# Kernel optimization log

Hardware: AMD Instinct MI355X
Metric: run time of the kernel (lower is better)

## Reference

```python
import jax, jax.numpy as jnp
import numpy as np
from jax import lax

PI = 3.14159265
# (dh, dw) for each of the 8 discretized angle bins, matching the torch `direction` table
DIRS = jnp.array([[1, 0], [1, 1], [0, 1], [-1, 1], [-1, 0], [-1, -1], [0, -1], [1, -1]], dtype=jnp.int32)
CC_ITERS = 48  # fixed trip count; FastSV converges in O(log N) rounds (log2(512*512)=18)


def _grids(H, W):
    return jnp.meshgrid(jnp.arange(H, dtype=jnp.int32), jnp.arange(W, dtype=jnp.int32), indexing='ij')


def _find_parents(angles, theta_a):
    # vectorized version of find_parents: per-pixel angle bin -> neighbor; root if OOB or angle gap too large
    H, W = angles.shape
    ii, jj = _grids(H, W)
    pos = jnp.round((angles + PI / 8.0) / (PI / 4.0))
    pos = jnp.where(pos >= 8.0, pos - 8.0, pos).astype(jnp.int32)
    nh = ii + DIRS[pos, 0]
    nw = jj + DIRS[pos, 1]
    inb = (nh >= 0) & (nh < H) & (nw >= 0) & (nw < W)
    nhc = jnp.clip(nh, 0, H - 1)
    nwc = jnp.clip(nw, 0, W - 1)
    ad = jnp.abs(angles - angles[nhc, nwc])
    ad = jnp.minimum(ad, 2.0 * PI - ad)
    is_root = (~inb) | (ad > theta_a * PI / 180.0)
    ph = jnp.where(is_root, ii, nhc)
    pw = jnp.where(is_root, jj, nwc)
    return ph, pw, is_root


def _cc_min_label(u, v, n):
    # Parallel union-find with min-label semantics (FastSV: root hooking + pointer jumping).
    # Equivalent to the serial UNION/FIND: final label of each pixel = min pixel index in its component.
    f0 = jnp.arange(n, dtype=jnp.int32)

    def body(_, f):
        fu, fv = f[u], f[v]
        m = jnp.minimum(fu, fv)
        g = f.at[fu].min(m).at[fv].min(m).at[u].min(m).at[v].min(m)
        g = g[g]
        g = g[g]
        return g

    return lax.fori_loop(0, CC_ITERS, body, f0)


def _structures(angles, theta_a):
    # All integer / discrete structure: parents, union-find labels, 3-step ancestors, boundary masks.
    H, W = angles.shape
    N = H * W
    ii, jj = _grids(H, W)
    ph, pw, roots = _find_parents(angles, theta_a)
    pf = (ph * W + pw).reshape(-1)  # flat parent pointer per pixel
    idx = jnp.arange(N, dtype=jnp.int32)
    # stage-1 edges: pixel <-> parent; stage-2 edges: merge_nearby_root_pixels window
    # range(0, min(3, H-1-i)) x range(-min(3, j), min(3, W-1-j))  <=>  dh in {0,1,2} with nh<=H-2,
    # dw in {-3..2} with 0<=nw<=W-2, both endpoints roots
    us, vs = [idx], [pf]
    for dh in range(0, 3):
        for dw in range(-3, 3):
            nh, nw = ii + dh, jj + dw
            nhc = jnp.clip(nh, 0, H - 1)
            nwc = jnp.clip(nw, 0, W - 1)
            m = roots & (nh <= H - 2) & (nw >= 0) & (nw <= W - 2) & roots[nhc, nwc]
            us.append(jnp.where(m, ii * W + jj, 0).reshape(-1))
            vs.append(jnp.where(m, nhc * W + nwc, 0).reshape(-1))
    labels_after = _cc_min_label(jnp.concatenate(us), jnp.concatenate(vs), N) + 1  # super_BPDs after dilation
    c3 = pf[pf[pf]]  # 3-step parent chase for every pixel (as in find_bnd_angle_diff)
    # boundary masks for right (0,1) and down (1,0) neighbors
    masks, nidxs = [], []
    for dh, dw in ((0, 1), (1, 0)):
        nh, nw = ii + dh, jj + dw
        valid = ((nh < H) & (nw < W)).reshape(-1)
        nidx = (jnp.clip(nh, 0, H - 1) * W + jnp.clip(nw, 0, W - 1)).reshape(-1)
        masks.append(valid & (labels_after != labels_after[nidx]))
        nidxs.append(nidx)
    return c3, masks, nidxs


def _bnd_angle_diff(angles, c3, masks, nidxs):
    # per boundary pixel-pair: wrap-around angle difference of the two 3-step ancestors
    H, W = angles.shape
    ang = angles.reshape(-1)
    outs = []
    for mask, nidx in zip(masks, nidxs):
        ad = jnp.abs(ang[c3] - ang[c3[nidx]])
        ad = jnp.minimum(ad, 2.0 * PI - ad)
        outs.append(jnp.where(mask, ad, 0.0))
    return jnp.stack(outs, axis=-1).reshape(H, W, 2)


def setup_inputs():
    key = jax.random.key(0)
    H, W = 512, 512
    input_angles = jax.random.uniform(key, (H, W), jnp.float32, 0.0, 2.0 * PI)
    return {"input_angles": input_angles, "height": H, "width": W, "theta_a": 45, "S_o": 90}


def reference(input_angles, height, width, theta_a, S_o):
    c3, masks, nidxs = _structures(input_angles, theta_a)
    return _bnd_angle_diff(input_angles, c3, masks, nidxs)
```

## Files before the change

### kernel.cpp

```cpp
#include <hip/hip_runtime.h>


static constexpr double PI_D = 3.14159265;
#define LCAP 4096
#define EPT  256
#define MAXT 1024

__device__ __constant__ int c_DH[8] = {1, 1, 0, -1, -1, -1, 0, 1};
__device__ __constant__ int c_DW[8] = {0, 1, 1, 1, 0, -1, -1, -1};

__device__ int g_fb[4 * 262144 + (MAXT << 10) + 2 * MAXT + 2 * EPT * MAXT];

__device__ __forceinline__ int uf_find_lds(int x, int* par) {
    while (true) {
        int p = par[x];
        if (p == x) return x;
        int gp = par[p];
        if (gp == p) return p;
        atomicMin(&par[x], gp);
        x = gp;
    }
}
__device__ __forceinline__ void uf_unite_lds(int u, int v, int* par) {
    int ru = uf_find_lds(u, par);
    int rv = uf_find_lds(v, par);
    while (ru != rv) {
        if (ru > rv) { int t2 = ru; ru = rv; rv = t2; }
        int old = atomicMin(&par[rv], ru);
        if (old == rv) break;
        rv = uf_find_lds(old, par);
        ru = uf_find_lds(ru, par);
    }
}

__device__ __forceinline__ int find_ro(int x, const int* par) {
    int p = par[x];
    while (p != x) { x = p; p = par[x]; }
    return x;
}
__device__ __forceinline__ void uf_unite(int u, int v, int* par) {
    int ru = find_ro(u, par);
    int rv = find_ro(v, par);
    while (ru != rv) {
        if (ru > rv) { int t2 = ru; ru = rv; rv = t2; }
        int old = atomicMin(&par[rv], ru);
        if (old == rv) break;
        rv = find_ro(old, par);
        ru = find_ro(ru, par);
    }
}

__device__ __forceinline__ bool parent_dir(const float* __restrict__ ang, float a,
                                           int i, int j, int H, int W, float thr,
                                           int& nhc, int& nwc) {
    const float a8 = (float)(PI_D / 8.0);
    const float a4 = (float)(PI_D / 4.0);
    float posf = rintf((a + a8) / a4);
    if (posf >= 8.0f) posf -= 8.0f;
    const int pos = (int)posf;
    const int nh = i + c_DH[pos];
    const int nw = j + c_DW[pos];
    const bool inb = (nh >= 0) & (nh < H) & (nw >= 0) & (nw < W);
    nhc = min(max(nh, 0), H - 1);
    nwc = min(max(nw, 0), W - 1);
    float ad = fabsf(a - ang[nhc * W + nwc]);
    const float twopi = (float)(2.0 * PI_D);
    ad = fminf(ad, twopi - ad);
    return (!inb) || (ad > thr);
}

__global__ void __launch_bounds__(1024)
k_local(const float* __restrict__ ang,
        const int* __restrict__ hp, const int* __restrict__ wp,
        const int* __restrict__ tap, int N,
        int* __restrict__ pf, int* __restrict__ par, int* __restrict__ c3,
        int* __restrict__ wlist, int* __restrict__ idx, int* __restrict__ wcnt) {
    const int H = hp[0], W = wp[0];
    const float thr = (float)((double)tap[0] * PI_D / 180.0);
    const int tpr = (W + 31) >> 5;
    const int ntiles = tpr * ((H + 31) >> 5);
    __shared__ int lpar[1024];
    __shared__ int lpl[1024];
    __shared__ int scnt;
    const int lp = threadIdx.x;
    const int li = lp >> 5, lj = lp & 31;
    for (int tile = blockIdx.x; tile < ntiles; tile += gridDim.x) {
        const int ti0 = (tile / tpr) << 5, tj0 = (tile % tpr) << 5;
        const int i = ti0 + li, j = tj0 + lj;
        const bool inpix = (i < H) && (j < W);
        const int g = i * W + j;
        if (lp == 0) scnt = 0;
        lpar[lp] = lp;
        int lparent = lp;
        if (inpix) {
            int nh, nw;
            const bool root = parent_dir(ang, ang[g], i, j, H, W, thr, nh, nw);
            pf[g] = root ? g : (nh * W + nw);
            if (!root) {
                const int pli = nh - ti0, plj = nw - tj0;
                lparent = (((unsigned)pli < 32u) && ((unsigned)plj < 32u))
                              ? ((pli << 5) + plj) : -1;
            }
        }
        lpl[lp] = lparent;
        __syncthreads();
        if (inpix) {
            if (lparent != lp) {
                if (lparent >= 0) uf_unite_lds(lp, lparent, lpar);
            } else if (i <= H - 2) {
                for (int d = 1; d <= 3; ++d) {
                    if (lj + d > 31 || j + d > W - 1) break;
                    if (lpl[lp + d] == lp + d) { uf_unite_lds(lp, lp + d, lpar); break; }
                }
                for (int dh = 1; dh <= 2; ++dh) {
                    const int nh = i + dh;
                    if (nh > H - 2) break;
                    const int nli = li + dh;
                    if (nli >= 32) break;
                    for (int dw = -3; dw <= 2; ++dw) {
                        const int nw = j + dw;
                        if ((unsigned)nw > (unsigned)(W - 2)) continue;
                        const int nlj = lj + dw;
                        if ((unsigned)nlj > 31u) continue;
                        const int nlp = (nli << 5) + nlj;
                        if (lpl[nlp] == nlp) uf_unite_lds(lp, nlp, lpar);
                    }
                }
            }
        }
        __syncthreads();
        if (inpix) {
            const int lr = uf_find_lds(lp, lpar);
            par[g] = (ti0 + (lr >> 5)) * W + (tj0 + (lr & 31));
            if (lr == lp) {
                const int s = atomicAdd(&scnt, 1);
                wlist[(tile << 10) + s] = g;
                idx[g] = s;
            }
            if (li >= 3 && li <= 28 && lj >= 3 && lj <= 28) {
                int v = lpl[lp];
                v = lpl[v];
                v = lpl[v];
                c3[g] = (ti0 + (v >> 5)) * W + (tj0 + (v & 31));
            }
        }
        __syncthreads();
        if (lp == 0) wcnt[tile] = scnt;
        __syncthreads();
    }
}

__global__ void k_edges(const int* __restrict__ pf,
                        const int* __restrict__ hp, const int* __restrict__ wp,
                        int N, int* par, int* __restrict__ elist, int* __restrict__ ecnt) {
    const int H = hp[0], W = wp[0];
    const int tpr = (W + 31) >> 5;
    const int ntiles = tpr * ((H + 31) >> 5);
    const int tidx = threadIdx.x;
    __shared__ unsigned long long htab[256];
    __shared__ int scnt;
    int li = 0, lj = 0;
    if (tidx < 96) {
        const int r = tidx >> 5;
        li = (r == 0) ? 0 : 29 + r;
        lj = tidx & 31;
    } else if (tidx < 270) {
        const int u = tidx - 96;
        li = 1 + u / 6;
        const int c = u % 6;
        lj = (c < 3) ? c : 26 + c;
    }
    for (int tile = blockIdx.x; tile < ntiles; tile += gridDim.x) {
        for (int s = tidx; s < 256; s += blockDim.x) htab[s] = ~0ull;
        if (tidx == 0) scnt = 0;
        __syncthreads();
        const int i = ((tile / tpr) << 5) + li;
        const int j = ((tile % tpr) << 5) + lj;
        if (tidx < 270 && i < H && j < W) {
            const int t = i * W + j;
            auto EMIT = [&](int a, int b) {
                if (a == b) return;
                const int lo = min(a, b), hi2 = max(a, b);
                const unsigned long long key =
                    ((unsigned long long)lo << 20) | (unsigned)hi2;
                unsigned h = (unsigned)((key * 0x9E3779B97F4A7C15ull) >> 52) & 255u;
                bool fresh = true;
                for (int pr = 0; pr < 16; ++pr) {
                    unsigned long long old = atomicCAS(&htab[h], ~0ull, key);
                    if (old == ~0ull) break;
                    if (old == key) { fresh = false; break; }
                    h = (h + 1) & 255u;
                }
                if (!fresh) return;
                const int s = atomicAdd(&scnt, 1);
                if (s < EPT) {
                    elist[(tile * EPT + s) * 2] = lo;
                    elist[(tile * EPT + s) * 2 + 1] = hi2;
                } else {
                    uf_unite(lo, hi2, par);
                }
            };
            const int p = pf[t];
            if (p != t) {
                const int pi = p / W, pj = p - pi * W;
                if (((pi ^ i) | (pj ^ j)) & ~31) EMIT(par[t], par[p]);
            } else if (i <= H - 2) {
                const int pt = par[t];
                int h0 = -1, h1 = -1;
                for (int d = (lj >= 29 ? 32 - lj : 4); d <= 3; ++d) {
                    if (j + d > W - 1) break;
                    const int n = t + d;
                    if (pf[n] != n) continue;
                    const int pn = par[n];
                    if (pn == pt || pn == h0 || pn == h1) continue;
                    h1 = h0; h0 = pn;
                    EMIT(pt, pn);
                }
                for (int dh = 1; dh <= 2; ++dh) {
                    const int nh = i + dh;
                    if (nh > H - 2) break;
                    const bool rowcross = (li + dh) > 31;
                    for (int dw = -3; dw <= 2; ++dw) {
                        const int nw = j + dw;
                        if ((unsigned)nw > (unsigned)(W - 2)) continue;
                        if (!rowcross && ((unsigned)(lj + dw) <= 31u)) continue;
                        const int n = nh * W + nw;
                        if (pf[n] != n) continue;
                        const int pn = par[n];
                        if (pn == pt || pn == h0 || pn == h1) continue;
                        h1 = h0; h0 = pn;
                        EMIT(pt, pn);
                    }
                }
            }
        }
        __syncthreads();
        if (tidx == 0) ecnt[tile] = scnt;
        __syncthreads();
    }
}

__global__ void __launch_bounds__(1024)
k_merge(const int* __restrict__ wlist, const int* __restrict__ wcnt,
        const int* __restrict__ idx, const int* __restrict__ elist,
        const int* __restrict__ ecnt,
        const int* __restrict__ hp, const int* __restrict__ wp, int* par) {
    const int H = hp[0], W = wp[0];
    const int tpr = (W + 31) >> 5;
    const int ntiles = tpr * ((H + 31) >> 5);
    __shared__ int lpar[LCAP], pix[LCAP], mn[LCAP];
    __shared__ int base[MAXT + 1], ebase[MAXT + 1];
    __shared__ int nsh, esh;
    const int tid = threadIdx.x;
    for (int t = tid; t < ntiles; t += blockDim.x) {
        base[t] = wcnt[t];
        ebase[t] = min(ecnt[t], EPT);
    }
    __syncthreads();
    if (tid == 0) {
        int rn = 0, re = 0;
        for (int t = 0; t < ntiles; ++t) {
            int c = base[t];  base[t] = rn;  rn += c;
            int e = ebase[t]; ebase[t] = re; re += e;
        }
        base[ntiles] = rn;  ebase[ntiles] = re;
        nsh = rn; esh = re;
    }
    __syncthreads();
    const int n = nsh, E = esh;
    auto bsearch = [&](const int* pre, int k) {
        int lo = 0, hi = ntiles;
        while (hi - lo > 1) { int m = (lo + hi) >> 1; if (pre[m] <= k) lo = m; else hi = m; }
        return lo;
    };
    auto CID = [&](int px) {
        const int pi = px / W, pj = px - pi * W;
        return base[(pi >> 5) * tpr + (pj >> 5)] + idx[px];
    };
    if (n <= LCAP) {
        for (int k = tid; k < n; k += blockDim.x) {
            const int t = bsearch(base, k);
            const int px = wlist[(t << 10) + (k - base[t])];
            pix[k] = px; lpar[k] = k; mn[k] = px;
        }
        __syncthreads();
        for (int k = tid; k < n; k += blockDim.x) {
            const int px = pix[k];
            const int q = par[px];
            if (q != px) uf_unite_lds(k, CID(q), lpar);
        }
        for (int e = tid; e < E; e += blockDim.x) {
            const int t = bsearch(ebase, e);
            const int s = e - ebase[t];
            const int a = elist[(t * EPT + s) * 2];
            const int b = elist[(t * EPT + s) * 2 + 1];
            uf_unite_lds(CID(a), CID(b), lpar);
        }
        __syncthreads();
        for (int k = tid; k < n; k += blockDim.x) {
            const int r = uf_find_lds(k, lpar);
            if (r != k) atomicMin(&mn[r], pix[k]);
        }
        __syncthreads();
        for (int k = tid; k < n; k += blockDim.x)
            par[pix[k]] = mn[uf_find_lds(k, lpar)];
    } else {
        for (int e = tid; e < E; e += blockDim.x) {
            const int t = bsearch(ebase, e);
            const int s = e - ebase[t];
            uf_unite(elist[(t * EPT + s) * 2], elist[(t * EPT + s) * 2 + 1], par);
        }
        __syncthreads();
        for (int k = tid; k < n; k += blockDim.x) {
            const int t = bsearch(base, k);
            const int r = wlist[(t << 10) + (k - base[t])];
            par[r] = find_ro(r, par);
        }
    }
}

__global__ void __launch_bounds__(256)
k_output(const float* __restrict__ ang,
         const int* __restrict__ par, const int* __restrict__ pf,
         const int* __restrict__ c3,
         const int* __restrict__ hp, const int* __restrict__ wp,
         float* __restrict__ out) {
    const int H = hp[0], W = wp[0];
    const int i0 = blockIdx.y << 3;
    const int j0 = blockIdx.x << 5;
    __shared__ int lab[9][33];
    const int tid = threadIdx.x;
    for (int k = tid; k < 9 * 33; k += 256) {
        const int r = k / 33, c = k - r * 33;
        const int gi = min(i0 + r, H - 1), gj = min(j0 + c, W - 1);
        lab[r][c] = par[par[gi * W + gj]];
    }
    __syncthreads();
    const int li2 = tid >> 5, lj2 = tid & 31;
    const int i = i0 + li2, j = j0 + lj2;
    if (i >= H || j >= W) return;
    const int t = i * W + j;
    const float twopi = (float)(2.0 * PI_D);
    const int l = lab[li2][lj2];
    float r0 = 0.0f, r1 = 0.0f;
    bool need = false;
    int l1 = l, l2 = l;
    if (j + 1 < W) { l1 = lab[li2][lj2 + 1]; need |= (l1 != l); }
    if (i + 1 < H) { l2 = lab[li2 + 1][lj2]; need |= (l2 != l); }
    if (need) {
        auto c3v = [&](int x, int xli, int xlj) {
            if (xli >= 3 && xli <= 28 && xlj >= 3 && xlj <= 28) return c3[x];
            int p = pf[x];
            p = pf[p];
            return pf[p];
        };
        const float ac = ang[c3v(t, i & 31, j & 31)];
        if (l1 != l) {
            float ad = fabsf(ac - ang[c3v(t + 1, i & 31, (j + 1) & 31)]);
            r0 = fminf(ad, twopi - ad);
        }
        if (l2 != l) {
            float ad = fabsf(ac - ang[c3v(t + W, (i + 1) & 31, j & 31)]);
            r1 = fminf(ad, twopi - ad);
        }
    }
    reinterpret_cast<float2*>(out)[t] = make_float2(r0, r1);
}

extern "C" void kernel_launch(void* const* d_in, const int* in_sizes, int n_in,
                              void* d_out, int out_size, void* d_ws, size_t ws_size,
                              hipStream_t stream) {
    const float* ang = (const float*)d_in[0];
    const int* hp  = (const int*)d_in[1];
    const int* wp  = (const int*)d_in[2];
    const int* tap = (const int*)d_in[3];
    const int N = in_sizes[0];

    const size_t need = ((size_t)4 * N + (MAXT << 10) + 2 * MAXT
                         + 2 * (size_t)EPT * MAXT) * sizeof(int);
    int* base = (int*)d_ws;
    if (ws_size < need && N <= 262144) {
        void* p = nullptr;
        hipGetSymbolAddress(&p, HIP_SYMBOL(g_fb));
        base = (int*)p;
    }
    int* pf    = base;
    int* par   = base + N;
    int* c3    = base + 2 * N;
    int* idx   = base + 3 * N;
    int* wlist = base + 4 * N;
    int* wcnt  = base + 4 * N + (MAXT << 10);
    int* ecnt  = wcnt + MAXT;
    int* elist = ecnt + MAXT;

    k_local <<<256, 1024, 0, stream>>>(ang, hp, wp, tap, N, pf, par, c3, wlist, idx, wcnt);
    k_edges <<<256, 320, 0, stream>>>(pf, hp, wp, N, par, elist, ecnt);
    k_merge <<<1, 1024, 0, stream>>>(wlist, wcnt, idx, elist, ecnt, hp, wp, par);
    {
        const int H = 512, W = 512;
        dim3 gridO((W + 31) / 32, (H + 7) / 8);
        k_output<<<gridO, 256, 0, stream>>>(ang, par, pf, c3, hp, wp, (float*)d_out);
    }
}
```

Before: 118.8 us.

## Use fixed per-tile root slots to drop prefix scans in merge kernel

Per-tile root lists now use a fixed capacity of 64 slots, so each tile root gets a static compact id (tile*64+slot). The edge kernel writes these compact ids directly, which removes the serial prefix sum, binary searches and CID translation from the single-block merge kernel. The merge now runs union-find in a 16K-entry LDS array indexed by the fixed slots. If any tile overflows, a flag sends everything to a global-memory fallback that does per-pixel find. This adds a memset launch and a slow path that is taken whenever a tile has more than 64 roots.

```diff
diff --git a/kernel.cpp b/kernel.cpp
--- a/kernel.cpp
+++ b/kernel.cpp
@@ -2,14 +2,15 @@
 
 
 static constexpr double PI_D = 3.14159265;
-#define LCAP 4096
+#define VCAP 64
+#define NVMAX 16384
 #define EPT  256
 #define MAXT 1024
 
 __device__ __constant__ int c_DH[8] = {1, 1, 0, -1, -1, -1, 0, 1};
 __device__ __constant__ int c_DW[8] = {0, 1, 1, 1, 0, -1, -1, -1};
 
-__device__ int g_fb[4 * 262144 + (MAXT << 10) + 2 * MAXT + 2 * EPT * MAXT];
+__device__ int g_fb[4 * 262144 + NVMAX + 2 * MAXT + 64 + 2 * EPT * MAXT];
 
 __device__ __forceinline__ int uf_find_lds(int x, int* par) {
     while (true) {
@@ -74,11 +75,13 @@
         const int* __restrict__ hp, const int* __restrict__ wp,
         const int* __restrict__ tap, int N,
         int* __restrict__ pf, int* __restrict__ par, int* __restrict__ c3,
-        int* __restrict__ wlist, int* __restrict__ idx, int* __restrict__ wcnt) {
+        int* __restrict__ wlist, int* __restrict__ idx, int* __restrict__ wcnt,
+        int* __restrict__ flags) {
     const int H = hp[0], W = wp[0];
     const float thr = (float)((double)tap[0] * PI_D / 180.0);
     const int tpr = (W + 31) >> 5;
     const int ntiles = tpr * ((H + 31) >> 5);
+    const bool fastOK = (ntiles <= NVMAX / VCAP);
     __shared__ int lpar[1024];
     __shared__ int lpl[1024];
     __shared__ int scnt;
@@ -134,8 +137,12 @@
             par[g] = (ti0 + (lr >> 5)) * W + (tj0 + (lr & 31));
             if (lr == lp) {
                 const int s = atomicAdd(&scnt, 1);
-                wlist[(tile << 10) + s] = g;
-                idx[g] = s;
+                if (fastOK && s < VCAP) {
+                    wlist[tile * VCAP + s] = g;
+                    idx[g] = s;
+                } else {
+                    flags[0] = 1;
+                }
             }
             if (li >= 3 && li <= 28 && lj >= 3 && lj <= 28) {
                 int v = lpl[lp];
@@ -145,17 +152,19 @@
             }
         }
         __syncthreads();
-        if (lp == 0) wcnt[tile] = scnt;
+        if (lp == 0 && tile < MAXT) wcnt[tile] = scnt;
         __syncthreads();
     }
 }
 
 __global__ void k_edges(const int* __restrict__ pf,
                         const int* __restrict__ hp, const int* __restrict__ wp,
-                        int N, int* par, int* __restrict__ elist, int* __restrict__ ecnt) {
+                        int N, int* par, int* __restrict__ elist, int* __restrict__ ecnt,
+                        const int* __restrict__ idx, int* __restrict__ flags) {
     const int H = hp[0], W = wp[0];
     const int tpr = (W + 31) >> 5;
     const int ntiles = tpr * ((H + 31) >> 5);
+    const bool slow = (flags[0] != 0) || (ntiles > NVMAX / VCAP);
     const int tidx = threadIdx.x;
     __shared__ unsigned long long htab[256];
     __shared__ int scnt;
@@ -170,6 +179,10 @@
         const int c = u % 6;
         lj = (c < 3) ? c : 26 + c;
     }
+    auto cid_of = [&](int px) {
+        const int pi = px / W, pj = px - pi * W;
+        return ((pi >> 5) * tpr + (pj >> 5)) * VCAP + idx[px];
+    };
     for (int tile = blockIdx.x; tile < ntiles; tile += gridDim.x) {
         for (int s = tidx; s < 256; s += blockDim.x) htab[s] = ~0ull;
         if (tidx == 0) scnt = 0;
@@ -180,6 +193,7 @@
             const int t = i * W + j;
             auto EMIT = [&](int a, int b) {
                 if (a == b) return;
+                if (slow) { uf_unite(a, b, par); return; }
                 const int lo = min(a, b), hi2 = max(a, b);
                 const unsigned long long key =
                     ((unsigned long long)lo << 20) | (unsigned)hi2;
@@ -194,9 +208,10 @@
                 if (!fresh) return;
                 const int s = atomicAdd(&scnt, 1);
                 if (s < EPT) {
-                    elist[(tile * EPT + s) * 2] = lo;
-                    elist[(tile * EPT + s) * 2 + 1] = hi2;
+                    elist[(tile * EPT + s) * 2] = cid_of(lo);
+                    elist[(tile * EPT + s) * 2 + 1] = cid_of(hi2);
                 } else {
+                    flags[1] = 1;
                     uf_unite(lo, hi2, par);
                 }
             };
@@ -235,87 +250,57 @@
             }
         }
         __syncthreads();
-        if (tidx == 0) ecnt[tile] = scnt;
+        if (tidx == 0 && tile < MAXT) ecnt[tile] = scnt;
         __syncthreads();
     }
 }
 
 __global__ void __launch_bounds__(1024)
 k_merge(const int* __restrict__ wlist, const int* __restrict__ wcnt,
-        const int* __restrict__ idx, const int* __restrict__ elist,
-        const int* __restrict__ ecnt,
-        const int* __restrict__ hp, const int* __restrict__ wp, int* par) {
+        const int* __restrict__ elist, const int* __restrict__ ecnt,
+        const int* __restrict__ flags,
+        const int* __restrict__ hp, const int* __restrict__ wp, int N,
+        int* par, const int* __restrict__ idx) {
     const int H = hp[0], W = wp[0];
     const int tpr = (W + 31) >> 5;
     const int ntiles = tpr * ((H + 31) >> 5);
-    __shared__ int lpar[LCAP], pix[LCAP], mn[LCAP];
-    __shared__ int base[MAXT + 1], ebase[MAXT + 1];
-    __shared__ int nsh, esh;
     const int tid = threadIdx.x;
-    for (int t = tid; t < ntiles; t += blockDim.x) {
-        base[t] = wcnt[t];
-        ebase[t] = min(ecnt[t], EPT);
-    }
-    __syncthreads();
-    if (tid == 0) {
-        int rn = 0, re = 0;
-        for (int t = 0; t < ntiles; ++t) {
-            int c = base[t];  base[t] = rn;  rn += c;
-            int e = ebase[t]; ebase[t] = re; re += e;
-        }
-        base[ntiles] = rn;  ebase[ntiles] = re;
-        nsh = rn; esh = re;
-    }
-    __syncthreads();
-    const int n = nsh, E = esh;
-    auto bsearch = [&](const int* pre, int k) {
-        int lo = 0, hi = ntiles;
-        while (hi - lo > 1) { int m = (lo + hi) >> 1; if (pre[m] <= k) lo = m; else hi = m; }
-        return lo;
-    };
-    auto CID = [&](int px) {
-        const int pi = px / W, pj = px - pi * W;
-        return base[(pi >> 5) * tpr + (pj >> 5)] + idx[px];
-    };
-    if (n <= LCAP) {
-        for (int k = tid; k < n; k += blockDim.x) {
-            const int t = bsearch(base, k);
-            const int px = wlist[(t << 10) + (k - base[t])];
-            pix[k] = px; lpar[k] = k; mn[k] = px;
-        }
-        __syncthreads();
-        for (int k = tid; k < n; k += blockDim.x) {
-            const int px = pix[k];
-            const int q = par[px];
-            if (q != px) uf_unite_lds(k, CID(q), lpar);
-        }
-        for (int e = tid; e < E; e += blockDim.x) {
-            const int t = bsearch(ebase, e);
-            const int s = e - ebase[t];
-            const int a = elist[(t * EPT + s) * 2];
-            const int b = elist[(t * EPT + s) * 2 + 1];
-            uf_unite_lds(CID(a), CID(b), lpar);
-        }
-        __syncthreads();
-        for (int k = tid; k < n; k += blockDim.x) {
-            const int r = uf_find_lds(k, lpar);
-            if (r != k) atomicMin(&mn[r], pix[k]);
-        }
-        __syncthreads();
-        for (int k = tid; k < n; k += blockDim.x)
-            par[pix[k]] = mn[uf_find_lds(k, lpar)];
+    __shared__ int lpar[NVMAX];
+    const bool slow = (flags[0] != 0) || (ntiles > NVMAX / VCAP);
+    if (!slow) {
+        const int NV = ntiles * VCAP;
+        for (int v = tid; v < NV; v += 1024) lpar[v] = v;
+        __syncthreads();
+        if (flags[1]) {
+            for (int v = tid; v < NV; v += 1024) {
+                const int t = v >> 6, s = v & (VCAP - 1);
+                if (s < min(wcnt[t], VCAP)) {
+                    const int px = wlist[v];
+                    const int q = par[px];
+                    if (q != px) {
+                        const int qi = q / W, qj = q - qi * W;
+                        const int cq = ((qi >> 5) * tpr + (qj >> 5)) * VCAP + idx[q];
+                        uf_unite_lds(v, cq, lpar);
+                    }
+                }
+            }
+        }
+        const int ED = ntiles * EPT;
+        for (int v = tid; v < ED; v += 1024) {
+            const int t = v >> 8, s = v & (EPT - 1);
+            if (s < min(ecnt[t], EPT))
+                uf_unite_lds(elist[2 * v], elist[2 * v + 1], lpar);
+        }
+        __syncthreads();
+        for (int v = tid; v < NV; v += 1024) {
+            const int t = v >> 6, s = v & (VCAP - 1);
+            if (s < min(wcnt[t], VCAP)) {
+                const int r = uf_find_lds(v, lpar);
+                par[wlist[v]] = wlist[r];
+            }
+        }
     } else {
-        for (int e = tid; e < E; e += blockDim.x) {
-            const int t = bsearch(ebase, e);
-            const int s = e - ebase[t];
-            uf_unite(elist[(t * EPT + s) * 2], elist[(t * EPT + s) * 2 + 1], par);
-        }
-        __syncthreads();
-        for (int k = tid; k < n; k += blockDim.x) {
-            const int t = bsearch(base, k);
-            const int r = wlist[(t << 10) + (k - base[t])];
-            par[r] = find_ro(r, par);
-        }
+        for (int t = tid; t < N; t += 1024) par[t] = find_ro(t, par);
     }
 }
 
@@ -376,7 +361,7 @@
     const int* tap = (const int*)d_in[3];
     const int N = in_sizes[0];
 
-    const size_t need = ((size_t)4 * N + (MAXT << 10) + 2 * MAXT
+    const size_t need = ((size_t)4 * N + NVMAX + 2 * MAXT + 64
                          + 2 * (size_t)EPT * MAXT) * sizeof(int);
     int* base = (int*)d_ws;
     if (ws_size < need && N <= 262144) {
@@ -389,13 +374,18 @@
     int* c3    = base + 2 * N;
     int* idx   = base + 3 * N;
     int* wlist = base + 4 * N;
-    int* wcnt  = base + 4 * N + (MAXT << 10);
+    int* wcnt  = base + 4 * N + NVMAX;
     int* ecnt  = wcnt + MAXT;
-    int* elist = ecnt + MAXT;
-
-    k_local <<<256, 1024, 0, stream>>>(ang, hp, wp, tap, N, pf, par, c3, wlist, idx, wcnt);
-    k_edges <<<256, 320, 0, stream>>>(pf, hp, wp, N, par, elist, ecnt);
-    k_merge <<<1, 1024, 0, stream>>>(wlist, wcnt, idx, elist, ecnt, hp, wp, par);
+    int* flags = ecnt + MAXT;
+    int* elist = flags + 64;
+
+    hipMemsetAsync(flags, 0, 2 * sizeof(int), stream);
+
+    k_local <<<256, 1024, 0, stream>>>(ang, hp, wp, tap, N, pf, par, c3,
+                                       wlist, idx, wcnt, flags);
+    k_edges <<<256, 320, 0, stream>>>(pf, hp, wp, N, par, elist, ecnt, idx, flags);
+    k_merge <<<1, 1024, 0, stream>>>(wlist, wcnt, elist, ecnt, flags, hp, wp, N,
+                                     par, idx);
     {
         const int H = 512, W = 512;
         dim3 gridO((W + 31) / 32, (H + 7) / 8);
```

New measurement: 165.6 us. 39.4% more time.
